# Kernel optimization log

Measured on AMD Instinct MI355X. Metric: run time of the kernel, lower is better.

Reference implementation:

```python
import jax, jax.numpy as jnp
import numpy as np

N = 50000   # nodes per domain graph
E = 800000  # edges per graph (avg degree 16)
IN = 512    # in_feats
H = 256     # n_hidden
C = 10      # n_classes
ALPHA = 1.0


def setup_inputs() -> dict:
    key = jax.random.key(0)
    ks = jax.random.split(key, 16)
    inp = {
        "features_s": jax.random.normal(ks[0], (N, IN), jnp.float32),
        "labels_s": jax.random.randint(ks[1], (N,), 0, C, jnp.int32),
        "features_t": jax.random.normal(ks[2], (N, IN), jnp.float32),
        "src_s": jax.random.randint(ks[3], (E,), 0, N, jnp.int32),
        "dst_s": jax.random.randint(ks[4], (E,), 0, N, jnp.int32),
        "src_t": jax.random.randint(ks[5], (E,), 0, N, jnp.int32),
        "dst_t": jax.random.randint(ks[6], (E,), 0, N, jnp.int32),
        # GraphConv layer 0: in_feats -> n_hidden (glorot-ish init)
        "W0": jax.random.normal(ks[7], (IN, H), jnp.float32) / np.float32(np.sqrt(IN)),
        "b0": jnp.zeros((H,), jnp.float32),
        # GraphConv layer 1: n_hidden -> n_hidden
        "W1": jax.random.normal(ks[8], (H, H), jnp.float32) / np.float32(np.sqrt(H)),
        "b1": jnp.zeros((H,), jnp.float32),
        # fc head: n_hidden -> n_classes
        "Wfc": jax.random.normal(ks[9], (H, C), jnp.float32) / np.float32(np.sqrt(H)),
        "bfc": jnp.zeros((C,), jnp.float32),
        # JS discriminator: (n_hidden*n_layers + n_classes) -> 2
        "Wd": jax.random.normal(ks[10], (H * 2 + C, 2), jnp.float32) / np.float32(np.sqrt(H * 2 + C)),
        "bd": jnp.zeros((2,), jnp.float32),
    }
    return inp


def _gconv(x, src, dst, W, b, n):
    # DGL GraphConv with norm='both': out = D_in^{-1/2} A D_out^{-1/2} x W + b, then relu.
    ones = jnp.ones(src.shape, x.dtype)
    deg_out = jax.ops.segment_sum(ones, src, num_segments=n)
    deg_in = jax.ops.segment_sum(ones, dst, num_segments=n)
    norm_src = jnp.maximum(deg_out, 1.0) ** -0.5   # [n]
    norm_dst = jnp.maximum(deg_in, 1.0) ** -0.5    # [n]
    h = (x * norm_src[:, None]) @ W                # [n, out] (mult-first: row scaling commutes)
    agg = jax.ops.segment_sum(h[src], dst, num_segments=n)  # gather-scatter SpMM
    return jax.nn.relu(agg * norm_dst[:, None] + b)


def reference(features_s, labels_s, features_t, src_s, dst_s, src_t, dst_t,
              W0, b0, W1, b1, Wfc, bfc, Wd, bd):
    # dropout omitted (eval-mode determinism)
    hs, ht = features_s, features_t
    s_list, t_list = [], []
    for (W, b) in ((W0, b0), (W1, b1)):
        hs = _gconv(hs, src_s, dst_s, W, b, N)
        ht = _gconv(ht, src_t, dst_t, W, b, N)
        s_list.append(hs)
        t_list.append(ht)
    logits_s = hs @ Wfc + bfc
    logits_t = ht @ Wfc + bfc
    s_list.append(logits_s)
    t_list.append(logits_t)

    # class loss: nll over log_softmax
    logp = jax.nn.log_softmax(logits_s, axis=-1)
    class_loss = -jnp.mean(jnp.take_along_axis(logp, labels_s[:, None].astype(jnp.int32), axis=1))

    # JS domain loss with gradient-reversal (identity in forward)
    s_f = jnp.concatenate(s_list, axis=1)  # [N, 2H+C]
    t_f = jnp.concatenate(t_list, axis=1)
    both = jnp.concatenate([s_f, t_f], axis=0)  # [2N, 2H+C]
    rev = -ALPHA * both + jax.lax.stop_gradient((1.0 + ALPHA) * both)  # GRL trick
    dlogits = rev @ Wd + bd
    dlogp = jax.nn.log_softmax(dlogits, axis=-1)
    dlabels = jnp.concatenate([jnp.zeros((N,), jnp.int32), jnp.ones((N,), jnp.int32)])
    domain_loss = -jnp.mean(jnp.take_along_axis(dlogp, dlabels[:, None], axis=1))

    return class_loss + 0.01 * domain_loss
```

## Files before the change

kernel.cpp:

```cpp
#include <hip/hip_runtime.h>
#include <cstdint>
#include <cstddef>

#define NN 50000
#define NNP 50016
#define EE 800000
#define INF 512
#define HH  256
#define CC  10
#define NB2 391
#define NTB 782
#define GB64 782
#define SPMM_BLOCKS 1600
#define HBIN 6250
#define HRNG 8
#define HSUB 32
#define SCAP 1536
#define ZROW NN

using bfrag = __attribute__((ext_vector_type(8))) __bf16;
using f32x4 = __attribute__((ext_vector_type(4))) float;

__device__ inline unsigned short f2bf(float x) {
    unsigned u = __builtin_bit_cast(unsigned, x);
    unsigned r = u + 0x7FFFu + ((u >> 16) & 1u);
    return (unsigned short)(r >> 16);
}
__device__ inline float bf2f(unsigned short h) {
    return __builtin_bit_cast(float, (unsigned)h << 16);
}

__device__ inline void gload_lds16(const void* gsrc, void* ldst) {
    __builtin_amdgcn_global_load_lds(
        (const __attribute__((address_space(1))) void*)gsrc,
        (__attribute__((address_space(3))) void*)ldst, 16, 0, 0);
}

template<int K>
__global__ void k_cast_wt(const float* __restrict__ W, ushort* __restrict__ Wt) {
    int idx = blockIdx.x * blockDim.x + threadIdx.x;
    if (idx >= K * HH) return;
    int n = idx / K, k = idx % K;
    Wt[idx] = f2bf(W[(size_t)k * HH + n]);
}

__global__ void k_cast_wtail(const float* __restrict__ Wfc, const float* __restrict__ Wd,
                             ushort* __restrict__ Wt1) {
    int idx = blockIdx.x * blockDim.x + threadIdx.x;
    if (idx >= 16 * HH) return;
    int n = idx >> 8, k = idx & 255;
    float v = 0.f;
    if (n < 10)       v = Wfc[(size_t)k * 10 + n];
    else if (n < 12)  v = Wd[(size_t)(HH + k) * 2 + (n - 10)];
    Wt1[idx] = f2bf(v);
}

__global__ void k_cast_wtail2(const float* __restrict__ Wd, ushort* __restrict__ Wt2) {
    int idx = blockIdx.x * blockDim.x + threadIdx.x;
    if (idx >= 16 * HH) return;
    int n = idx >> 8, k = idx & 255;
    float v = (n < 2) ? Wd[(size_t)k * 2 + n] : 0.f;
    Wt2[idx] = f2bf(v);
}

__global__ __launch_bounds__(256) void k_deghist(
        const int* __restrict__ src_s, const int* __restrict__ dst_s,
        const int* __restrict__ src_t, const int* __restrict__ dst_t,
        ushort* __restrict__ pcnt) {
    __shared__ int hist[HBIN];
    const int task = blockIdx.x >> 5;
    const int sub  = blockIdx.x & 31;
    const int arr = task >> 3, range = task & 7;
    const int* p = (arr == 0) ? src_s : (arr == 1) ? dst_s : (arr == 2) ? src_t : dst_t;
    const int4* p4 = reinterpret_cast<const int4*>(p);
    const int lo = range * HBIN;
    for (int j = threadIdx.x; j < HBIN; j += 256) hist[j] = 0;
    __syncthreads();
    for (int i = sub * 256 + (int)threadIdx.x; i < EE / 4; i += HSUB * 256) {
        int4 v = p4[i];
        int a0 = v.x - lo, a1 = v.y - lo, a2 = v.z - lo, a3 = v.w - lo;
        if ((unsigned)a0 < (unsigned)HBIN) atomicAdd(&hist[a0], 1);
        if ((unsigned)a1 < (unsigned)HBIN) atomicAdd(&hist[a1], 1);
        if ((unsigned)a2 < (unsigned)HBIN) atomicAdd(&hist[a2], 1);
        if ((unsigned)a3 < (unsigned)HBIN) atomicAdd(&hist[a3], 1);
    }
    __syncthreads();
    ushort* out = pcnt + ((size_t)task * HSUB + sub) * HBIN;
    for (int j = threadIdx.x; j < HBIN; j += 256) out[j] = (ushort)hist[j];
}

__global__ void k_degsum(const ushort* __restrict__ pcnt, int* __restrict__ cnt) {
    int g = blockIdx.x * blockDim.x + threadIdx.x;
    if (g >= 4 * NN) return;
    int arr = g / NN;
    int node = g - arr * NN;
    int range = node / HBIN;
    int j = node - range * HBIN;
    const ushort* p = pcnt + ((size_t)(arr * HRNG + range) * HSUB) * HBIN + j;
    int s = 0;
    #pragma unroll
    for (int k = 0; k < HSUB; ++k) s += p[(size_t)k * HBIN];
    cnt[g] = s;
}

__global__ void k_scan_blk(const int* __restrict__ cnt, int* __restrict__ off,
                           int* __restrict__ btot) {
    __shared__ int wsum[4];
    int tid = threadIdx.x, lane = tid & 63, wid = tid >> 6;
    int i = blockIdx.x * 256 + tid;
    int v = 0;
    if (i < 2 * NN) v = (i < NN) ? cnt[NN + i] : cnt[2 * NN + i];
    int s = v;
    #pragma unroll
    for (int o = 1; o < 64; o <<= 1) {
        int t = __shfl_up(s, o, 64);
        if (lane >= o) s += t;
    }
    if (lane == 63) wsum[wid] = s;
    __syncthreads();
    if (tid == 0) {
        int a = 0;
        #pragma unroll
        for (int w2 = 0; w2 < 4; ++w2) { int t = wsum[w2]; wsum[w2] = a; a += t; }
        btot[blockIdx.x] = a;
    }
    __syncthreads();
    if (i < 2 * NN) off[i] = wsum[wid] + s - v;
}

__global__ void k_scan_tops(const int* __restrict__ btot, int* __restrict__ bbase,
                            int* __restrict__ off) {
    __shared__ int wsum[8];
    int tid = threadIdx.x, lane = tid & 63, wid = tid >> 6;
    int v = (tid < NB2) ? btot[tid] : 0;
    int s = v;
    #pragma unroll
    for (int o = 1; o < 64; o <<= 1) {
        int t = __shfl_up(s, o, 64);
        if (lane >= o) s += t;
    }
    if (lane == 63) wsum[wid] = s;
    __syncthreads();
    if (tid == 0) {
        int a = 0;
        #pragma unroll
        for (int w2 = 0; w2 < 8; ++w2) { int t = wsum[w2]; wsum[w2] = a; a += t; }
        off[2 * NN] = a;
    }
    __syncthreads();
    if (tid < NB2) bbase[tid] = wsum[wid] + s - v;
}

__global__ void k_scan_fin(int* __restrict__ off, const int* __restrict__ bbase,
                           const int* __restrict__ cnt,
                           float* __restrict__ ns, float* __restrict__ nd,
                           ushort* __restrict__ y2) {
    if (blockIdx.x == 0) {
        #pragma unroll
        for (int j = 0; j < 2; ++j) {
            int idx = j * 256 + (int)threadIdx.x;
            int gg = idx >> 8, grp = (idx >> 5) & 7, c = idx & 31;
            y2[(((size_t)gg * 8 + grp) * NNP + ZROW) * 32 + c] = 0;
        }
    }
    int i = blockIdx.x * blockDim.x + threadIdx.x;
    if (i >= 2 * NN) return;
    int o = off[i] + bbase[i >> 8];
    off[i] = o;
    int co = (i < NN) ? cnt[i] : cnt[NN + i];
    int ci = (i < NN) ? cnt[NN + i] : cnt[2 * NN + i];
    ns[i] = 1.0f / sqrtf(fmaxf((float)co, 1.0f));
    nd[i] = 1.0f / sqrtf(fmaxf((float)ci, 1.0f));
}

__global__ void k_degpos(const ushort* __restrict__ pcnt, const int* __restrict__ off,
                         int* __restrict__ base2) {
    int i = blockIdx.x * blockDim.x + threadIdx.x;
    if (i >= 2 * NN) return;
    int g = (i < NN) ? 0 : 1;
    int node = i - g * NN;
    int range = node / HBIN;
    int bin = node - range * HBIN;
    int arr = g ? 3 : 1;
    const ushort* p = pcnt + ((size_t)(arr * HRNG + range) * HSUB) * HBIN + bin;
    int* b = base2 + ((size_t)(g * HRNG + range) * HSUB) * HBIN + bin;
    int run = off[i];
    #pragma unroll
    for (int s = 0; s < HSUB; ++s) {
        b[(size_t)s * HBIN] = run;
        run += p[(size_t)s * HBIN];
    }
}

__global__ __launch_bounds__(256) void k_fill3(
        const int* __restrict__ src_s, const int* __restrict__ dst_s,
        const int* __restrict__ src_t, const int* __restrict__ dst_t,
        const int* __restrict__ base2, int* __restrict__ csr_src) {
    __shared__ int cur[HBIN];
    const int combo = blockIdx.x & 15;
    const int sub = blockIdx.x >> 4;
    const int g = combo >> 3, range = combo & 7;
    const int4* d4 = reinterpret_cast<const int4*>(g ? dst_t : dst_s);
    const int4* s4 = reinterpret_cast<const int4*>(g ? src_t : src_s);
    const int lo = range * HBIN;
    const int* b = base2 + (size_t)combo * HSUB * HBIN + (size_t)sub * HBIN;
    for (int j = threadIdx.x; j < HBIN; j += 256) cur[j] = b[j];
    __syncthreads();
    for (int i = sub * 256 + (int)threadIdx.x; i < EE / 4; i += HSUB * 256) {
        int4 d = d4[i];
        int b0 = d.x - lo, b1 = d.y - lo, b2 = d.z - lo, b3 = d.w - lo;
        bool o0 = (unsigned)b0 < (unsigned)HBIN;
        bool o1 = (unsigned)b1 < (unsigned)HBIN;
        bool o2 = (unsigned)b2 < (unsigned)HBIN;
        bool o3 = (unsigned)b3 < (unsigned)HBIN;
        if (o0 | o1 | o2 | o3) {
            int4 s = s4[i];
            if (o0) csr_src[atomicAdd(&cur[b0], 1)] = s.x;
            if (o1) csr_src[atomicAdd(&cur[b1], 1)] = s.y;
            if (o2) csr_src[atomicAdd(&cur[b2], 1)] = s.z;
            if (o3) csr_src[atomicAdd(&cur[b3], 1)] = s.w;
        }
    }
}

template<int K, bool F32A>
__global__ __launch_bounds__(256, 4) void k_gemm2(
        const void* __restrict__ Ap_s, const void* __restrict__ Ap_t,
        const ushort* __restrict__ Bt, const float* __restrict__ ns2,
        ushort* __restrict__ y2) {
    __shared__ ushort As[64 * 64];
    __shared__ ushort Bs[256 * 64];
    const int g = blockIdx.x >= GB64 ? 1 : 0;
    const void* Ap = g ? Ap_t : Ap_s;
    const float* ns = ns2 + (size_t)g * NN;
    ushort* y2g = y2 + (size_t)g * 8 * NNP * 32;
    const int m0 = (blockIdx.x - g * GB64) * 64;
    const int t = threadIdx.x;
    const int wid = t >> 6, lane = t & 63;
    const int wc = wid * 64;
    const int l15 = lane & 15, lg = lane >> 4;

    f32x4 acc[4][4];
    #pragma unroll
    for (int m = 0; m < 4; ++m)
        #pragma unroll
        for (int n = 0; n < 4; ++n)
            acc[m][n] = {0.f, 0.f, 0.f, 0.f};

    const int srow = t >> 3;
    const int schunk = t & 7;

    for (int k0 = 0; k0 < K; k0 += 64) {
        if constexpr (F32A) {
            #pragma unroll
            for (int i = 0; i < 2; ++i) {
                int row = srow + i * 32;
                int sw = ((schunk ^ (row & 7)) * 8);
                int m = m0 + row; if (m >= NN) m = NN - 1;
                const float* ap = (const float*)Ap + (size_t)m * K + k0 + schunk * 8;
                float4 f0 = *reinterpret_cast<const float4*>(ap);
                float4 f1 = *reinterpret_cast<const float4*>(ap + 4);
                uint4 va;
                va.x = (unsigned)f2bf(f0.x) | ((unsigned)f2bf(f0.y) << 16);
                va.y = (unsigned)f2bf(f0.z) | ((unsigned)f2bf(f0.w) << 16);
                va.z = (unsigned)f2bf(f1.x) | ((unsigned)f2bf(f1.y) << 16);
                va.w = (unsigned)f2bf(f1.z) | ((unsigned)f2bf(f1.w) << 16);
                *reinterpret_cast<uint4*>(&As[row * 64 + sw]) = va;
            }
        } else {
            #pragma unroll
            for (int i = 0; i < 2; ++i) {
                int row = srow + i * 32;
                int sw = ((schunk ^ (row & 7)) * 8);
                int m = m0 + row; if (m >= NN) m = NN - 1;
                const ushort* gsrc = (const ushort*)Ap + (size_t)m * K + k0 + sw;
                gload_lds16(gsrc, &As[(size_t)(wid * 8 + i * 32) * 64]);
            }
        }
        #pragma unroll
        for (int i = 0; i < 8; ++i) {
            int row = srow + i * 32;
            int sw = ((schunk ^ (row & 7)) * 8);
            const ushort* gsrc = &Bt[(size_t)row * K + k0 + sw];
            gload_lds16(gsrc, &Bs[(size_t)(wid * 8 + i * 32) * 64]);
        }
        __syncthreads();
        #pragma unroll
        for (int kk = 0; kk < 64; kk += 32) {
            const int kc = kk >> 3;
            bfrag af[4];
            #pragma unroll
            for (int m = 0; m < 4; ++m) {
                int row = m * 16 + l15;
                af[m] = *reinterpret_cast<const bfrag*>(&As[row * 64 + (((lg + kc) ^ (row & 7)) * 8)]);
            }
            #pragma unroll
            for (int n = 0; n < 4; ++n) {
                int row = wc + n * 16 + l15;
                bfrag bg = *reinterpret_cast<const bfrag*>(&Bs[row * 64 + (((lg + kc) ^ (row & 7)) * 8)]);
                #pragma unroll
                for (int m = 0; m < 4; ++m)
                    acc[m][n] = __builtin_amdgcn_mfma_f32_16x16x32_bf16(af[m], bg, acc[m][n], 0, 0, 0);
            }
        }
        __syncthreads();
    }

    ushort* tile = Bs;
    #pragma unroll
    for (int m = 0; m < 4; ++m) {
        #pragma unroll
        for (int r = 0; r < 4; ++r) {
            int rloc = m * 16 + lg * 4 + r;
            int rowg = m0 + rloc;
            float nsv = ns[rowg < NN ? rowg : NN - 1];
            #pragma unroll
            for (int n = 0; n < 4; ++n) {
                int col = wc + n * 16 + l15;
                int blk = (col >> 3) ^ (rloc & 7);
                tile[rloc * 256 + (blk << 3) + (col & 7)] = f2bf(acc[m][n][r] * nsv);
            }
        }
    }
    __syncthreads();
    {
        int row = t >> 2, sub = t & 3;
        int m = m0 + row;
        if (m < NN) {
            #pragma unroll
            for (int grp = 0; grp < 8; ++grp) {
                int blk = (grp * 4 + sub) ^ (row & 7);
                uint4 v = *reinterpret_cast<const uint4*>(&tile[row * 256 + (blk << 3)]);
                *reinterpret_cast<uint4*>(&y2g[((size_t)grp * NNP + m) * 32 + sub * 8]) = v;
            }
        }
    }
}

__device__ inline void add8(float* a, uint4 v) {
    a[0] += __builtin_bit_cast(float, v.x << 16);
    a[1] += __builtin_bit_cast(float, v.x & 0xffff0000u);
    a[2] += __builtin_bit_cast(float, v.y << 16);
    a[3] += __builtin_bit_cast(float, v.y & 0xffff0000u);
    a[4] += __builtin_bit_cast(float, v.z << 16);
    a[5] += __builtin_bit_cast(float, v.z & 0xffff0000u);
    a[6] += __builtin_bit_cast(float, v.w << 16);
    a[7] += __builtin_bit_cast(float, v.w & 0xffff0000u);
}

__global__ __launch_bounds__(256) void k_spmm6(
        const ushort* __restrict__ y2, const int* __restrict__ off,
        const int* __restrict__ csr_src, const float* __restrict__ nd_arr,
        const float* __restrict__ bias, ushort* __restrict__ h_out) {
    __shared__ int sidx[4][SCAP];
    const int grp = blockIdx.x & 7;
    const int blk = blockIdx.x >> 3;
    const int tid = threadIdx.x;
    const int lane = tid & 63, wid = tid >> 6;
    const int slot = lane >> 2;
    const int sub = lane & 3;
    const ushort* ybase = y2 + (size_t)grp * NNP * 32 + sub * 8;

    const int nb = (blk * 4 + wid) * 64;
    int s_wave0 = 0, cnt = 0;
    if (nb < NN) {
        int nend = nb + 64 < NN ? nb + 64 : NN;
        s_wave0 = off[nb];
        cnt = off[nend] - s_wave0;
    }
    int stage = cnt < SCAP ? cnt : SCAP;
    for (int j = lane; j < stage; j += 64)
        sidx[wid][j] = csr_src[s_wave0 + j];
    __syncthreads();

    float bia[8];
    #pragma unroll
    for (int j = 0; j < 8; ++j) bia[j] = bias[grp * 32 + sub * 8 + j];

    int e0[4], e1[4];
    float a[4][8];
    #pragma unroll
    for (int c = 0; c < 4; ++c) {
        int n = nb + c * 16 + slot;
        bool v = n < NN;
        e0[c] = v ? off[n] - s_wave0 : 0;
        e1[c] = v ? off[n + 1] - s_wave0 : 0;
        #pragma unroll
        for (int j = 0; j < 8; ++j) a[c][j] = 0.f;
    }
    int tmax = max(max(e1[0] - e0[0], e1[1] - e0[1]), max(e1[2] - e0[2], e1[3] - e0[3]));

    if (cnt <= SCAP) {
        for (int t = 0; t < tmax; t += 2) {
            uint4 v[8];
            #pragma unroll
            for (int u = 0; u < 2; ++u)
                #pragma unroll
                for (int c = 0; c < 4; ++c) {
                    int ec = e0[c] + t + u;
                    bool val = ec < e1[c];
                    int ecc = val ? ec : 0;
                    int id = sidx[wid][ecc];
                    id = val ? id : ZROW;
                    v[u * 4 + c] = *reinterpret_cast<const uint4*>(&ybase[(size_t)id * 32]);
                }
            #pragma unroll
            for (int u = 0; u < 2; ++u)
                #pragma unroll
                for (int c = 0; c < 4; ++c) add8(a[c], v[u * 4 + c]);
        }
    } else {
        for (int t = 0; t < tmax; t += 2) {
            uint4 v[8];
            #pragma unroll
            for (int u = 0; u < 2; ++u)
                #pragma unroll
                for (int c = 0; c < 4; ++c) {
                    int ec = e0[c] + t + u;
                    bool val = ec < e1[c];
                    int ecc = val ? ec : 0;
                    int id = csr_src[s_wave0 + ecc];
                    id = val ? id : ZROW;
                    v[u * 4 + c] = *reinterpret_cast<const uint4*>(&ybase[(size_t)id * 32]);
                }
            #pragma unroll
            for (int u = 0; u < 2; ++u)
                #pragma unroll
                for (int c = 0; c < 4; ++c) add8(a[c], v[u * 4 + c]);
        }
    }

    #pragma unroll
    for (int c = 0; c < 4; ++c) {
        int n = nb + c * 16 + slot;
        if (n >= NN) continue;
        float nd = nd_arr[n];
        ushort r[8];
        #pragma unroll
        for (int j = 0; j < 8; ++j) r[j] = f2bf(fmaxf(a[c][j] * nd + bia[j], 0.f));
        uint4 pk;
        pk.x = (unsigned)r[0] | ((unsigned)r[1] << 16);
        pk.y = (unsigned)r[2] | ((unsigned)r[3] << 16);
        pk.z = (unsigned)r[4] | ((unsigned)r[5] << 16);
        pk.w = (unsigned)r[6] | ((unsigned)r[7] << 16);
        *reinterpret_cast<uint4*>(&h_out[(size_t)n * 256 + grp * 32 + sub * 8]) = pk;
    }
}

__global__ __launch_bounds__(256) void k_tail_mfma(
        const ushort* __restrict__ h0s, const ushort* __restrict__ h0t,
        const ushort* __restrict__ h1s, const ushort* __restrict__ h1t,
        const ushort* __restrict__ Wt1, const ushort* __restrict__ Wt2,
        const float* __restrict__ bfc, const float* __restrict__ bd,
        const int* __restrict__ labels,
        float* __restrict__ pcls, float* __restrict__ pdom) {
    __shared__ float sT1[4][16][17];
    __shared__ float sT2[4][16][17];
    __shared__ float sc[4], sd[4];
    const int g = blockIdx.x >= NTB ? 1 : 0;
    const int bi = blockIdx.x - g * NTB;
    const ushort* h0 = g ? h0t : h0s;
    const ushort* h1 = g ? h1t : h1s;
    const int tid = threadIdx.x;
    const int wid = tid >> 6, lane = tid & 63;
    const int l15 = lane & 15, lg = lane >> 4;
    const int base = bi * 64 + wid * 16;

    int arow = base + l15; if (arow >= NN) arow = NN - 1;
    const ushort* a1 = h1 + (size_t)arow * 256 + lg * 8;
    const ushort* a0 = h0 + (size_t)arow * 256 + lg * 8;
    const ushort* b1 = Wt1 + (size_t)l15 * 256 + lg * 8;
    const ushort* b2 = Wt2 + (size_t)l15 * 256 + lg * 8;
    f32x4 acc1 = {0.f, 0.f, 0.f, 0.f};
    f32x4 acc2 = {0.f, 0.f, 0.f, 0.f};
    #pragma unroll
    for (int kk = 0; kk < 8; ++kk) {
        bfrag af1 = *reinterpret_cast<const bfrag*>(a1 + kk * 32);
        bfrag bg1 = *reinterpret_cast<const bfrag*>(b1 + kk * 32);
        acc1 = __builtin_amdgcn_mfma_f32_16x16x32_bf16(af1, bg1, acc1, 0, 0, 0);
        bfrag af0 = *reinterpret_cast<const bfrag*>(a0 + kk * 32);
        bfrag bg2 = *reinterpret_cast<const bfrag*>(b2 + kk * 32);
        acc2 = __builtin_amdgcn_mfma_f32_16x16x32_bf16(af0, bg2, acc2, 0, 0, 0);
    }
    #pragma unroll
    for (int j = 0; j < 4; ++j) {
        sT1[wid][lg * 4 + j][l15] = acc1[j];
        sT2[wid][lg * 4 + j][l15] = acc2[j];
    }
    __syncthreads();

    float cls = 0.f, dom = 0.f;
    int n = base + lane;
    if (lane < 16 && n < NN) {
        float lgt[10];
        #pragma unroll
        for (int c = 0; c < 10; ++c) lgt[c] = sT1[wid][lane][c] + bfc[c];
        float dl0 = bd[0] + sT2[wid][lane][0] + sT1[wid][lane][10];
        float dl1 = bd[1] + sT2[wid][lane][1] + sT1[wid][lane][11];
        if (g == 0) {
            float m = lgt[0];
            #pragma unroll
            for (int c = 1; c < 10; ++c) m = fmaxf(m, lgt[c]);
            float s = 0.f;
            #pragma unroll
            for (int c = 0; c < 10; ++c) s += expf(lgt[c] - m);
            int lab = labels[n];
            float tgt = lgt[0];
            #pragma unroll
            for (int c = 1; c < 10; ++c) tgt = (c == lab) ? lgt[c] : tgt;
            cls = -(tgt - (m + logf(s)));
        }
        float m2 = fmaxf(dl0, dl1);
        float lse2 = m2 + logf(expf(dl0 - m2) + expf(dl1 - m2));
        dom = -((g ? dl1 : dl0) - lse2);
    }
    #pragma unroll
    for (int o = 1; o < 16; o <<= 1) {
        cls += __shfl_xor(cls, o, 64);
        dom += __shfl_xor(dom, o, 64);
    }
    if (lane == 0) { sc[wid] = cls; sd[wid] = dom; }
    __syncthreads();
    if (tid == 0) {
        float c = sc[0] + sc[1] + sc[2] + sc[3];
        float d = sd[0] + sd[1] + sd[2] + sd[3];
        if (g == 0) pcls[bi] = c;
        pdom[g * NTB + bi] = d;
    }
}

__global__ void k_finalize(const float* __restrict__ pcls, const float* __restrict__ pdom,
                           float* __restrict__ out) {
    __shared__ float sc[4], sd[4];
    int tid = threadIdx.x, lane = tid & 63, wid = tid >> 6;
    float c = 0.f, d = 0.f;
    for (int i = tid; i < NTB; i += 256) c += pcls[i];
    for (int i = tid; i < 2 * NTB; i += 256) d += pdom[i];
    #pragma unroll
    for (int o = 32; o; o >>= 1) {
        c += __shfl_xor(c, o, 64);
        d += __shfl_xor(d, o, 64);
    }
    if (lane == 0) { sc[wid] = c; sd[wid] = d; }
    __syncthreads();
    if (tid == 0) {
        float ct = sc[0] + sc[1] + sc[2] + sc[3];
        float dt = sd[0] + sd[1] + sd[2] + sd[3];
        out[0] = ct / (float)NN + 0.01f * (dt / (float)(2 * NN));
    }
}

extern "C" void kernel_launch(void* const* d_in, const int* in_sizes, int n_in,
                              void* d_out, int out_size, void* d_ws, size_t ws_size,
                              hipStream_t stream) {
    const float* features_s = (const float*)d_in[0];
    const int*   labels_s   = (const int*)d_in[1];
    const float* features_t = (const float*)d_in[2];
    const int*   src_s      = (const int*)d_in[3];
    const int*   dst_s      = (const int*)d_in[4];
    const int*   src_t      = (const int*)d_in[5];
    const int*   dst_t      = (const int*)d_in[6];
    const float* W0         = (const float*)d_in[7];
    const float* b0         = (const float*)d_in[8];
    const float* W1         = (const float*)d_in[9];
    const float* b1         = (const float*)d_in[10];
    const float* Wfc        = (const float*)d_in[11];
    const float* bfc        = (const float*)d_in[12];
    const float* Wd         = (const float*)d_in[13];
    const float* bd         = (const float*)d_in[14];
    float* out = (float*)d_out;

    auto align256 = [](size_t x) { return (x + 255) & ~(size_t)255; };
    char* w = (char*)d_ws;
    ushort* h0s    = (ushort*)w; w += align256((size_t)NN * HH * 2);
    ushort* h0t    = (ushort*)w; w += align256((size_t)NN * HH * 2);
    ushort* h1s    = (ushort*)w; w += align256((size_t)NN * HH * 2);
    ushort* h1t    = (ushort*)w; w += align256((size_t)NN * HH * 2);
    ushort* y2     = (ushort*)w; w += align256((size_t)2 * 8 * NNP * 32 * 2);
    ushort* W0t    = (ushort*)w; w += align256((size_t)INF * HH * 2);
    ushort* W1t    = (ushort*)w; w += align256((size_t)HH * HH * 2);
    ushort* Wt1    = (ushort*)w; w += align256((size_t)16 * HH * 2);
    ushort* Wt2    = (ushort*)w; w += align256((size_t)16 * HH * 2);
    float* ns      = (float*)w;  w += align256((size_t)2 * NN * 4);
    float* nd      = (float*)w;  w += align256((size_t)2 * NN * 4);
    int*   cnt     = (int*)w;    w += align256((size_t)4 * NN * 4);
    int*   csr_off = (int*)w;    w += align256((size_t)(2 * NN + 1) * 4);
    int*   csr_src = (int*)w;    w += align256((size_t)2 * EE * 4);
    int*   btot    = (int*)w;    w += align256((size_t)NB2 * 4);
    int*   bbase   = (int*)w;    w += align256((size_t)NB2 * 4);
    float* pcls    = (float*)w;  w += align256((size_t)NTB * 4);
    float* pdom    = (float*)w;  w += align256((size_t)2 * NTB * 4);
    ushort* pcnt   = (ushort*)w; w += align256((size_t)4 * HRNG * HSUB * HBIN * 2);
    int*   base2   = (int*)w;    w += align256((size_t)2 * HRNG * HSUB * HBIN * 4);

    const int TB = 256;
    k_cast_wt<INF><<<(INF * HH + TB - 1) / TB, TB, 0, stream>>>(W0, W0t);
    k_cast_wt<HH><<<(HH * HH + TB - 1) / TB, TB, 0, stream>>>(W1, W1t);
    k_cast_wtail<<<(16 * HH + TB - 1) / TB, TB, 0, stream>>>(Wfc, Wd, Wt1);
    k_cast_wtail2<<<(16 * HH + TB - 1) / TB, TB, 0, stream>>>(Wd, Wt2);

    k_deghist<<<4 * HRNG * HSUB, TB, 0, stream>>>(src_s, dst_s, src_t, dst_t, pcnt);
    k_degsum<<<(4 * NN + TB - 1) / TB, TB, 0, stream>>>(pcnt, cnt);
    k_scan_blk<<<NB2, TB, 0, stream>>>(cnt, csr_off, btot);
    k_scan_tops<<<1, 512, 0, stream>>>(btot, bbase, csr_off);
    k_scan_fin<<<NB2, TB, 0, stream>>>(csr_off, bbase, cnt, ns, nd, y2);
    k_degpos<<<NB2, TB, 0, stream>>>(pcnt, csr_off, base2);
    k_fill3<<<16 * HSUB, TB, 0, stream>>>(src_s, dst_s, src_t, dst_t, base2, csr_src);

    const int* off_s = csr_off;
    const int* off_t = csr_off + NN;
    ushort* y2s = y2;
    ushort* y2t = y2 + (size_t)8 * NNP * 32;

    k_gemm2<INF, true><<<2 * GB64, TB, 0, stream>>>(features_s, features_t, W0t, ns, y2);
    k_spmm6<<<SPMM_BLOCKS, TB, 0, stream>>>(y2s, off_s, csr_src, nd, b0, h0s);
    k_spmm6<<<SPMM_BLOCKS, TB, 0, stream>>>(y2t, off_t, csr_src, nd + NN, b0, h0t);

    k_gemm2<HH, false><<<2 * GB64, TB, 0, stream>>>(h0s, h0t, W1t, ns, y2);
    k_spmm6<<<SPMM_BLOCKS, TB, 0, stream>>>(y2s, off_s, csr_src, nd, b1, h1s);
    k_spmm6<<<SPMM_BLOCKS, TB, 0, stream>>>(y2t, off_t, csr_src, nd + NN, b1, h1t);

    k_tail_mfma<<<2 * NTB, TB, 0, stream>>>(h0s, h0t, h1s, h1t, Wt1, Wt2, bfc, bd,
                                            labels_s, pcls, pdom);
    k_finalize<<<1, TB, 0, stream>>>(pcls, pdom, out);
}
```

Baseline: 430.7 us.

## Double-buffer LDS tiles in k_gemm2 to overlap global loads with MFMA

```diff
diff --git a/kernel.cpp b/kernel.cpp
--- a/kernel.cpp
+++ b/kernel.cpp
@@ -224,12 +224,12 @@
 }
 
 template<int K, bool F32A>
-__global__ __launch_bounds__(256, 4) void k_gemm2(
+__global__ __launch_bounds__(256, 2) void k_gemm2(
         const void* __restrict__ Ap_s, const void* __restrict__ Ap_t,
         const ushort* __restrict__ Bt, const float* __restrict__ ns2,
         ushort* __restrict__ y2) {
-    __shared__ ushort As[64 * 64];
-    __shared__ ushort Bs[256 * 64];
+    __shared__ ushort As[2][64 * 64];
+    __shared__ ushort Bs[2][256 * 64];
     const int g = blockIdx.x >= GB64 ? 1 : 0;
     const void* Ap = g ? Ap_t : Ap_s;
     const float* ns = ns2 + (size_t)g * NN;
@@ -249,42 +249,77 @@
 
     const int srow = t >> 3;
     const int schunk = t & 7;
-
-    for (int k0 = 0; k0 < K; k0 += 64) {
-        if constexpr (F32A) {
-            #pragma unroll
-            for (int i = 0; i < 2; ++i) {
+    constexpr int NT = K / 64;
+
+    if constexpr (F32A) {
+        #pragma unroll
+        for (int i = 0; i < 2; ++i) {
+            int row = srow + i * 32;
+            int sw = ((schunk ^ (row & 7)) * 8);
+            int m = m0 + row; if (m >= NN) m = NN - 1;
+            const float* ap = (const float*)Ap + (size_t)m * K + schunk * 8;
+            float4 f0 = *reinterpret_cast<const float4*>(ap);
+            float4 f1 = *reinterpret_cast<const float4*>(ap + 4);
+            uint4 va;
+            va.x = (unsigned)f2bf(f0.x) | ((unsigned)f2bf(f0.y) << 16);
+            va.y = (unsigned)f2bf(f0.z) | ((unsigned)f2bf(f0.w) << 16);
+            va.z = (unsigned)f2bf(f1.x) | ((unsigned)f2bf(f1.y) << 16);
+            va.w = (unsigned)f2bf(f1.z) | ((unsigned)f2bf(f1.w) << 16);
+            *reinterpret_cast<uint4*>(&As[0][row * 64 + sw]) = va;
+        }
+    } else {
+        #pragma unroll
+        for (int i = 0; i < 2; ++i) {
+            int row = srow + i * 32;
+            int sw = ((schunk ^ (row & 7)) * 8);
+            int m = m0 + row; if (m >= NN) m = NN - 1;
+            gload_lds16((const ushort*)Ap + (size_t)m * K + sw,
+                        &As[0][(size_t)(wid * 8 + i * 32) * 64]);
+        }
+    }
+    #pragma unroll
+    for (int i = 0; i < 8; ++i) {
+        int row = srow + i * 32;
+        int sw = ((schunk ^ (row & 7)) * 8);
+        gload_lds16(&Bt[(size_t)row * K + sw],
+                    &Bs[0][(size_t)(wid * 8 + i * 32) * 64]);
+    }
+    __syncthreads();
+
+    for (int tix = 0; tix < NT; ++tix) {
+        const int cur = tix & 1;
+        const int nxt = cur ^ 1;
+        const bool more = (tix + 1 < NT);
+        const int k0n = (tix + 1) * 64;
+        float4 fa0[2], fa1[2];
+        if (more) {
+            if constexpr (F32A) {
+                #pragma unroll
+                for (int i = 0; i < 2; ++i) {
+                    int row = srow + i * 32;
+                    int m = m0 + row; if (m >= NN) m = NN - 1;
+                    const float* ap = (const float*)Ap + (size_t)m * K + k0n + schunk * 8;
+                    fa0[i] = *reinterpret_cast<const float4*>(ap);
+                    fa1[i] = *reinterpret_cast<const float4*>(ap + 4);
+                }
+            } else {
+                #pragma unroll
+                for (int i = 0; i < 2; ++i) {
+                    int row = srow + i * 32;
+                    int sw = ((schunk ^ (row & 7)) * 8);
+                    int m = m0 + row; if (m >= NN) m = NN - 1;
+                    gload_lds16((const ushort*)Ap + (size_t)m * K + k0n + sw,
+                                &As[nxt][(size_t)(wid * 8 + i * 32) * 64]);
+                }
+            }
+            #pragma unroll
+            for (int i = 0; i < 8; ++i) {
                 int row = srow + i * 32;
                 int sw = ((schunk ^ (row & 7)) * 8);
-                int m = m0 + row; if (m >= NN) m = NN - 1;
-                const float* ap = (const float*)Ap + (size_t)m * K + k0 + schunk * 8;
-                float4 f0 = *reinterpret_cast<const float4*>(ap);
-                float4 f1 = *reinterpret_cast<const float4*>(ap + 4);
-                uint4 va;
-                va.x = (unsigned)f2bf(f0.x) | ((unsigned)f2bf(f0.y) << 16);
-                va.y = (unsigned)f2bf(f0.z) | ((unsigned)f2bf(f0.w) << 16);
-                va.z = (unsigned)f2bf(f1.x) | ((unsigned)f2bf(f1.y) << 16);
-                va.w = (unsigned)f2bf(f1.z) | ((unsigned)f2bf(f1.w) << 16);
-                *reinterpret_cast<uint4*>(&As[row * 64 + sw]) = va;
+                gload_lds16(&Bt[(size_t)row * K + k0n + sw],
+                            &Bs[nxt][(size_t)(wid * 8 + i * 32) * 64]);
             }
-        } else {
-            #pragma unroll
-            for (int i = 0; i < 2; ++i) {
-                int row = srow + i * 32;
-                int sw = ((schunk ^ (row & 7)) * 8);
-                int m = m0 + row; if (m >= NN) m = NN - 1;
-                const ushort* gsrc = (const ushort*)Ap + (size_t)m * K + k0 + sw;
-                gload_lds16(gsrc, &As[(size_t)(wid * 8 + i * 32) * 64]);
-            }
-        }
-        #pragma unroll
-        for (int i = 0; i < 8; ++i) {
-            int row = srow + i * 32;
-            int sw = ((schunk ^ (row & 7)) * 8);
-            const ushort* gsrc = &Bt[(size_t)row * K + k0 + sw];
-            gload_lds16(gsrc, &Bs[(size_t)(wid * 8 + i * 32) * 64]);
-        }
-        __syncthreads();
+        }
         #pragma unroll
         for (int kk = 0; kk < 64; kk += 32) {
             const int kc = kk >> 3;
@@ -292,21 +327,36 @@
             #pragma unroll
             for (int m = 0; m < 4; ++m) {
                 int row = m * 16 + l15;
-                af[m] = *reinterpret_cast<const bfrag*>(&As[row * 64 + (((lg + kc) ^ (row & 7)) * 8)]);
+                af[m] = *reinterpret_cast<const bfrag*>(&As[cur][row * 64 + (((lg + kc) ^ (row & 7)) * 8)]);
             }
             #pragma unroll
             for (int n = 0; n < 4; ++n) {
                 int row = wc + n * 16 + l15;
-                bfrag bg = *reinterpret_cast<const bfrag*>(&Bs[row * 64 + (((lg + kc) ^ (row & 7)) * 8)]);
+                bfrag bg = *reinterpret_cast<const bfrag*>(&Bs[cur][row * 64 + (((lg + kc) ^ (row & 7)) * 8)]);
                 #pragma unroll
                 for (int m = 0; m < 4; ++m)
                     acc[m][n] = __builtin_amdgcn_mfma_f32_16x16x32_bf16(af[m], bg, acc[m][n], 0, 0, 0);
             }
         }
+        if (more) {
+            if constexpr (F32A) {
+                #pragma unroll
+                for (int i = 0; i < 2; ++i) {
+                    int row = srow + i * 32;
+                    int sw = ((schunk ^ (row & 7)) * 8);
+                    uint4 va;
+                    va.x = (unsigned)f2bf(fa0[i].x) | ((unsigned)f2bf(fa0[i].y) << 16);
+                    va.y = (unsigned)f2bf(fa0[i].z) | ((unsigned)f2bf(fa0[i].w) << 16);
+                    va.z = (unsigned)f2bf(fa1[i].x) | ((unsigned)f2bf(fa1[i].y) << 16);
+                    va.w = (unsigned)f2bf(fa1[i].z) | ((unsigned)f2bf(fa1[i].w) << 16);
+                    *reinterpret_cast<uint4*>(&As[nxt][row * 64 + sw]) = va;
+                }
+            }
+        }
         __syncthreads();
     }
 
-    ushort* tile = Bs;
+    ushort* tile = &Bs[0][0];
     #pragma unroll
     for (int m = 0; m < 4; ++m) {
         #pragma unroll
```

Result: slower. 453.2 us (+5.2%).
